# Performance work log

Hardware: AMD Instinct MI355X
Metric: run time of the kernel (lower is better)

The kernel has to match this reference:

```python
import jax, jax.numpy as jnp
import numpy as np

B, S, D = 8, 4096, 1024
MINR, MAXR = 0.9, 0.999


def setup_inputs() -> dict:
    key = jax.random.key(0)
    ks = jax.random.split(key, 10)

    def dense(k, fin, fout):
        # lecun_normal-style init for flax nn.Dense kernels
        return jax.random.normal(k, (fin, fout), jnp.float32) * (fin ** -0.5)

    x = jax.random.normal(ks[0], (B, S, D), jnp.float32)
    # RNN 'a' param: stable_init -> uniform in [min_rad, max_rad]
    a_fwd = jax.random.uniform(ks[1], (D,), jnp.float32, MINR, MAXR)
    # RGLRU 'a' param: recurrence_init
    u = jax.random.uniform(ks[2], (D,), jnp.float32)
    log_rad = 0.5 * jnp.log(u * (MAXR ** 2 - MINR ** 2) + MINR ** 2)
    a_param = jnp.log(jnp.exp(-log_rad) - 1.0)
    return {
        "x": x,
        "a_fwd": a_fwd,
        "Wf1": dense(ks[3], D, D), "bf1": jnp.zeros((D,), jnp.float32),
        "Wf2": dense(ks[4], D, D), "bf2": jnp.zeros((D,), jnp.float32),
        "Wbx": dense(ks[5], D, D), "bbx": jnp.zeros((D,), jnp.float32),
        "Wgx": dense(ks[6], D, D), "bgx": jnp.zeros((D,), jnp.float32),
        "Wga": dense(ks[7], D, D), "bga": jnp.zeros((D,), jnp.float32),
        "a_param": a_param,
        "Wb2": dense(ks[8], D, D), "bb2": jnp.zeros((D,), jnp.float32),
    }


def reference(x, a_fwd, Wf1, bf1, Wf2, bf2, Wbx, bbx, Wgx, bgx, Wga, bga,
              a_param, Wb2, bb2):
    b = x.shape[0]
    d = Wf1.shape[1]
    identity = x
    xg = jax.nn.gelu(x)  # flax nn.gelu default = tanh approximation

    # ---- forward branch: plain linear RNN  h = a*h + x_t ----
    u = xg @ Wf1 + bf1                       # [B,S,D]
    u_sf = jnp.swapaxes(u, 0, 1)             # [S,B,D]

    def step_f(h, ut):
        h = a_fwd * h + ut
        return h, h

    _, hf = jax.lax.scan(step_f, jnp.zeros((b, d), u.dtype), u_sf)
    out_f = jnp.swapaxes(hf, 0, 1) @ Wf2 + bf2

    # ---- backward branch: RG-LRU, reversed scan ----
    v = xg @ Wbx + bbx                       # [B,S,D]
    gate_x = jax.nn.sigmoid(v @ Wgx + bgx)
    gate_a = jax.nn.sigmoid(v @ Wga + bga)
    log_a = -8.0 * gate_a * jax.nn.softplus(a_param)
    a = jnp.exp(log_a)                       # [B,S,D]
    # h = a*h + sqrt(1 - a^2) * (gate_x * v)
    scaled_in = jnp.sqrt(1.0 - jnp.exp(2.0 * log_a)) * (gate_x * v)

    a_sf = jnp.swapaxes(a, 0, 1)             # [S,B,D]
    in_sf = jnp.swapaxes(scaled_in, 0, 1)    # [S,B,D]

    def step_b(h, inp):
        a_t, g_t = inp
        h = a_t * h + g_t
        return h, h

    _, hb = jax.lax.scan(step_b, jnp.zeros((b, d), v.dtype), (a_sf, in_sf),
                         reverse=True)
    out_b = jnp.swapaxes(hb, 0, 1) @ Wb2 + bb2

    return out_f + out_b + identity
```

## Files before the change

### kernel.cpp

```cpp
#include <hip/hip_runtime.h>

typedef __bf16 bf16;
typedef __bf16 bf16x8 __attribute__((ext_vector_type(8)));
typedef float floatx4 __attribute__((ext_vector_type(4)));

typedef __attribute__((address_space(1))) const void gvoid_t;
typedef __attribute__((address_space(3))) void lvoid_t;

#define B_DIM 8
#define S_DIM 4096
#define M_DIM 32768
#define CHUNK 128
#define NCHUNK 32

__device__ __forceinline__ void gload_lds16(const bf16* g, bf16* l) {
    __builtin_amdgcn_global_load_lds((gvoid_t*)g, (lvoid_t*)l, 16, 0, 0);
}

__device__ __forceinline__ float gelu_tanh(float x) {
    float x3 = x * x * x;
    return 0.5f * x * (1.0f + tanhf(0.7978845608028654f * (x + 0.044715f * x3)));
}

__device__ __forceinline__ float sigmoidf(float z) {
    return 1.0f / (1.0f + expf(-z));
}

__global__ void prep_weights(const float* __restrict__ W0, const float* __restrict__ W1,
                             const float* __restrict__ W2, const float* __restrict__ W3,
                             const float* __restrict__ W4, const float* __restrict__ W5,
                             bf16* __restrict__ T0, bf16* __restrict__ T1,
                             bf16* __restrict__ T2, bf16* __restrict__ T3,
                             bf16* __restrict__ T4, bf16* __restrict__ T5) {
    __shared__ float tile[32][33];
    int mz = blockIdx.z;
    const float* W = mz == 0 ? W0 : mz == 1 ? W1 : mz == 2 ? W2 : mz == 3 ? W3 : mz == 4 ? W4 : W5;
    bf16* T = mz == 0 ? T0 : mz == 1 ? T1 : mz == 2 ? T2 : mz == 3 ? T3 : mz == 4 ? T4 : T5;
    int tn = blockIdx.x * 32;
    int tk = blockIdx.y * 32;
    int tx = threadIdx.x & 31, ty = threadIdx.x >> 5;
#pragma unroll
    for (int i = 0; i < 4; ++i)
        tile[ty + i * 8][tx] = W[(size_t)(tk + ty + i * 8) * 1024 + tn + tx];
    __syncthreads();
#pragma unroll
    for (int i = 0; i < 4; ++i)
        T[(size_t)(tn + ty + i * 8) * 1024 + tk + tx] = (bf16)tile[tx][ty + i * 8];
}

__global__ void sp_kernel(const float* __restrict__ a_param, float* __restrict__ spbuf) {
    int d = blockIdx.x * 256 + threadIdx.x;
    spbuf[d] = log1pf(expf(a_param[d]));
}

__global__ void gelu_kernel(const float* __restrict__ x, bf16* __restrict__ xg) {
    size_t i = (size_t)blockIdx.x * 256 + threadIdx.x;
    float4 v = ((const float4*)x)[i];
    bf16 o0 = (bf16)gelu_tanh(v.x), o1 = (bf16)gelu_tanh(v.y);
    bf16 o2 = (bf16)gelu_tanh(v.z), o3 = (bf16)gelu_tanh(v.w);
    typedef __bf16 bf16x4 __attribute__((ext_vector_type(4)));
    bf16x4 o = {o0, o1, o2, o3};
    ((bf16x4*)xg)[i] = o;
}

template <int MODE>
__launch_bounds__(256, 2)
__global__ void gemm_k1024(const bf16* __restrict__ A, const bf16* __restrict__ Bt,
                           float* __restrict__ outf, bf16* __restrict__ outh,
                           const float* __restrict__ bias,
                           const float* __restrict__ auxf,
                           const bf16* __restrict__ labuf,
                           const bf16* __restrict__ vbuf,
                           const float* __restrict__ bias2) {
    __shared__ __align__(16) bf16 lsA[128 * 64];
    __shared__ __align__(16) bf16 lsB[128 * 64];
    const int tid = threadIdx.x;
    const int wave = tid >> 6;
    const int lane = tid & 63;
    const int lane15 = lane & 15;
    const int quad = lane >> 4;
    const int wm = wave & 1, wn = wave >> 1;
    const int blk = blockIdx.x;
    const int xcd = blk & 7;
    const int j = blk >> 3;
    const long m0 = (long)(xcd * 32 + (j >> 3)) * 128;
    const long n0 = (long)(j & 7) * 128;
    const int r_in = lane >> 3;
    const int cch = lane & 7;

    floatx4 acc[4][4] = {};

    for (int kt = 0; kt < 16; ++kt) {
        __syncthreads();
#pragma unroll
        for (int i = 0; i < 4; ++i) {
            int rr = (i * 4 + wave) * 8 + r_in;
            int g = cch ^ (rr & 7);
            gload_lds16(A + (size_t)(m0 + rr) * 1024 + kt * 64 + g * 8, &lsA[(i * 4 + wave) * 512]);
            gload_lds16(Bt + (size_t)(n0 + rr) * 1024 + kt * 64 + g * 8, &lsB[(i * 4 + wave) * 512]);
        }
        __syncthreads();
#pragma unroll
        for (int kk = 0; kk < 2; ++kk) {
            bf16x8 af[4], bfr[4];
#pragma unroll
            for (int mi = 0; mi < 4; ++mi) {
                int ml = wm * 64 + mi * 16 + lane15;
                af[mi] = *(const bf16x8*)&lsA[ml * 64 + ((kk * 4 + quad) ^ (ml & 7)) * 8];
            }
#pragma unroll
            for (int ni = 0; ni < 4; ++ni) {
                int nl = wn * 64 + ni * 16 + lane15;
                bfr[ni] = *(const bf16x8*)&lsB[nl * 64 + ((kk * 4 + quad) ^ (nl & 7)) * 8];
            }
#pragma unroll
            for (int mi = 0; mi < 4; ++mi)
#pragma unroll
                for (int ni = 0; ni < 4; ++ni)
                    acc[mi][ni] = __builtin_amdgcn_mfma_f32_16x16x32_bf16(af[mi], bfr[ni], acc[mi][ni], 0, 0, 0);
        }
    }

#pragma unroll
    for (int mi = 0; mi < 4; ++mi) {
#pragma unroll
        for (int ni = 0; ni < 4; ++ni) {
            floatx4 v = acc[mi][ni];
            long gn = n0 + wn * 64 + ni * 16 + lane15;
#pragma unroll
            for (int r = 0; r < 4; ++r) {
                long gm = m0 + wm * 64 + mi * 16 + quad * 4 + r;
                size_t o = (size_t)gm * 1024 + gn;
                if (MODE == 0) {
                    outf[o] = v[r] + bias[gn];
                } else if (MODE == 1) {
                    outh[o] = (bf16)(v[r] + bias[gn]);
                } else if (MODE == 2) {
                    float z = v[r] + bias[gn];
                    outh[o] = (bf16)(-8.0f * sigmoidf(z) * auxf[gn]);
                } else if (MODE == 3) {
                    float z = v[r] + bias[gn];
                    float laf = (float)labuf[o];
                    float sc = sqrtf(-expm1f(2.0f * laf)) * sigmoidf(z) * (float)vbuf[o];
                    outh[o] = (bf16)sc;
                } else if (MODE == 4) {
                    outf[o] = v[r] + bias[gn] + bias2[gn] + auxf[o];
                } else {
                    outf[o] += v[r];
                }
            }
        }
    }
}

__global__ void fscan1(const float* __restrict__ u, const float* __restrict__ a_fwd,
                       float* __restrict__ carry) {
    int d = (blockIdx.x & 3) * 256 + threadIdx.x;
    int c = (blockIdx.x >> 2) & 31;
    int b = blockIdx.x >> 7;
    float a = a_fwd[d];
    const float* up = u + ((size_t)(b * S_DIM + c * CHUNK)) * 1024 + d;
    float h = 0.0f;
#pragma unroll 8
    for (int t = 0; t < CHUNK; ++t) h = fmaf(a, h, up[(size_t)t * 1024]);
    carry[((size_t)c * 8 + b) * 1024 + d] = h;
}
__global__ void fscan2(const float* __restrict__ carry, const float* __restrict__ a_fwd,
                       float* __restrict__ H) {
    int idx = blockIdx.x * 256 + threadIdx.x;
    int d = idx & 1023, b = idx >> 10;
    float a = a_fwd[d];
    float aL = a;
#pragma unroll
    for (int i = 0; i < 7; ++i) aL *= aL;
    float h = 0.0f;
    for (int c = 0; c < NCHUNK; ++c) {
        size_t o = ((size_t)c * 8 + b) * 1024 + d;
        H[o] = h;
        h = fmaf(aL, h, carry[o]);
    }
}
__global__ void fscan3(const float* __restrict__ u, const float* __restrict__ a_fwd,
                       const float* __restrict__ H, bf16* __restrict__ hf) {
    int d = (blockIdx.x & 3) * 256 + threadIdx.x;
    int c = (blockIdx.x >> 2) & 31;
    int b = blockIdx.x >> 7;
    float a = a_fwd[d];
    const float* up = u + ((size_t)(b * S_DIM + c * CHUNK)) * 1024 + d;
    bf16* op = hf + ((size_t)(b * S_DIM + c * CHUNK)) * 1024 + d;
    float h = H[((size_t)c * 8 + b) * 1024 + d];
#pragma unroll 4
    for (int t = 0; t < CHUNK; ++t) {
        h = fmaf(a, h, up[(size_t)t * 1024]);
        op[(size_t)t * 1024] = (bf16)h;
    }
}

__global__ void bscan1(const bf16* __restrict__ la, const bf16* __restrict__ sc,
                       float* __restrict__ BL, float* __restrict__ BP) {
    int d = (blockIdx.x & 3) * 256 + threadIdx.x;
    int c = (blockIdx.x >> 2) & 31;
    int b = blockIdx.x >> 7;
    const bf16* lap = la + ((size_t)(b * S_DIM + c * CHUNK)) * 1024 + d;
    const bf16* gp = sc + ((size_t)(b * S_DIM + c * CHUNK)) * 1024 + d;
    float h = 0.0f, slog = 0.0f;
#pragma unroll 4
    for (int t = CHUNK - 1; t >= 0; --t) {
        float laf = (float)lap[(size_t)t * 1024];
        h = fmaf(expf(laf), h, (float)gp[(size_t)t * 1024]);
        slog += laf;
    }
    size_t o = ((size_t)c * 8 + b) * 1024 + d;
    BL[o] = h;
    BP[o] = expf(slog);
}
__global__ void bscan2(const float* __restrict__ BL, const float* __restrict__ BP,
                       float* __restrict__ R) {
    int idx = blockIdx.x * 256 + threadIdx.x;
    int d = idx & 1023, b = idx >> 10;
    float r = 0.0f;
    for (int c = NCHUNK - 1; c >= 0; --c) {
        size_t o = ((size_t)c * 8 + b) * 1024 + d;
        R[o] = r;
        r = fmaf(BP[o], r, BL[o]);
    }
}
__global__ void bscan3(const bf16* __restrict__ la, const bf16* __restrict__ sc,
                       const float* __restrict__ R, bf16* __restrict__ hb) {
    int d = (blockIdx.x & 3) * 256 + threadIdx.x;
    int c = (blockIdx.x >> 2) & 31;
    int b = blockIdx.x >> 7;
    const bf16* lap = la + ((size_t)(b * S_DIM + c * CHUNK)) * 1024 + d;
    const bf16* gp = sc + ((size_t)(b * S_DIM + c * CHUNK)) * 1024 + d;
    bf16* op = hb + ((size_t)(b * S_DIM + c * CHUNK)) * 1024 + d;
    float h = R[((size_t)c * 8 + b) * 1024 + d];
#pragma unroll 4
    for (int t = CHUNK - 1; t >= 0; --t) {
        h = fmaf(expf((float)lap[(size_t)t * 1024]), h, (float)gp[(size_t)t * 1024]);
        op[(size_t)t * 1024] = (bf16)h;
    }
}

extern "C" void kernel_launch(void* const* d_in, const int* in_sizes, int n_in,
                              void* d_out, int out_size, void* d_ws, size_t ws_size,
                              hipStream_t stream) {
    const float* x       = (const float*)d_in[0];
    const float* a_fwd   = (const float*)d_in[1];
    const float* Wf1     = (const float*)d_in[2];
    const float* bf1     = (const float*)d_in[3];
    const float* Wf2     = (const float*)d_in[4];
    const float* bf2     = (const float*)d_in[5];
    const float* Wbx     = (const float*)d_in[6];
    const float* bbx     = (const float*)d_in[7];
    const float* Wgx     = (const float*)d_in[8];
    const float* bgx     = (const float*)d_in[9];
    const float* Wga     = (const float*)d_in[10];
    const float* bga     = (const float*)d_in[11];
    const float* a_param = (const float*)d_in[12];
    const float* Wb2     = (const float*)d_in[13];
    const float* bb2     = (const float*)d_in[14];
    float* out = (float*)d_out;
    (void)in_sizes; (void)n_in; (void)out_size; (void)ws_size;

    char* ws = (char*)d_ws;
    size_t off = 0;
    const size_t WSZ = (size_t)1024 * 1024 * 2;
    bf16* Wf1t = (bf16*)(ws + off); off += WSZ;
    bf16* Wbxt = (bf16*)(ws + off); off += WSZ;
    bf16* Wgxt = (bf16*)(ws + off); off += WSZ;
    bf16* Wgat = (bf16*)(ws + off); off += WSZ;
    bf16* Wf2t = (bf16*)(ws + off); off += WSZ;
    bf16* Wb2t = (bf16*)(ws + off); off += WSZ;
    float* spbuf = (float*)(ws + off); off += 4096;
    const size_t BSZ = (size_t)M_DIM * 1024 * 2;
    bf16* buf0 = (bf16*)(ws + off); off += BSZ;
    bf16* buf1 = (bf16*)(ws + off); off += BSZ;
    bf16* buf2 = (bf16*)(ws + off); off += BSZ;
    float* Fc = (float*)(ws + off); off += (size_t)NCHUNK * 8 * 1024 * 4;
    float* FH = (float*)(ws + off); off += (size_t)NCHUNK * 8 * 1024 * 4;
    float* BL = (float*)(ws + off); off += (size_t)NCHUNK * 8 * 1024 * 4;
    float* BP = (float*)(ws + off); off += (size_t)NCHUNK * 8 * 1024 * 4;
    float* BR = (float*)(ws + off); off += (size_t)NCHUNK * 8 * 1024 * 4;

    bf16* xg = buf0;
    bf16* hf = buf0;
    bf16* vb = buf1;
    bf16* hb = buf1;
    bf16* la = buf2;
    float* u = (float*)d_out;
    bf16* sc = (bf16*)d_out;

    prep_weights<<<dim3(32, 32, 6), 256, 0, stream>>>(Wf1, Wbx, Wgx, Wga, Wf2, Wb2,
                                                      Wf1t, Wbxt, Wgxt, Wgat, Wf2t, Wb2t);
    sp_kernel<<<4, 256, 0, stream>>>(a_param, spbuf);
    gelu_kernel<<<32768, 256, 0, stream>>>(x, xg);
    gemm_k1024<0><<<2048, 256, 0, stream>>>(xg, Wf1t, u, nullptr, bf1, nullptr, nullptr, nullptr, nullptr);
    gemm_k1024<1><<<2048, 256, 0, stream>>>(xg, Wbxt, nullptr, vb, bbx, nullptr, nullptr, nullptr, nullptr);
    fscan1<<<1024, 256, 0, stream>>>(u, a_fwd, Fc);
    fscan2<<<32, 256, 0, stream>>>(Fc, a_fwd, FH);
    fscan3<<<1024, 256, 0, stream>>>(u, a_fwd, FH, hf);
    gemm_k1024<2><<<2048, 256, 0, stream>>>(vb, Wgat, nullptr, la, bga, spbuf, nullptr, nullptr, nullptr);
    gemm_k1024<3><<<2048, 256, 0, stream>>>(vb, Wgxt, nullptr, sc, bgx, nullptr, la, vb, nullptr);
    bscan1<<<1024, 256, 0, stream>>>(la, sc, BL, BP);
    bscan2<<<32, 256, 0, stream>>>(BL, BP, BR);
    bscan3<<<1024, 256, 0, stream>>>(la, sc, BR, hb);
    gemm_k1024<4><<<2048, 256, 0, stream>>>(hf, Wf2t, out, nullptr, bf2, x, nullptr, nullptr, bb2);
    gemm_k1024<5><<<2048, 256, 0, stream>>>(hb, Wb2t, out, nullptr, nullptr, nullptr, nullptr, nullptr, nullptr);
}
```

Baseline: 954.5 us.

## Replace GEMM with 256x256-tile, 8-wave, double-buffered prefetching kernel

All six bf16 GEMMs now use a new kernel with 256x256 output tiles and 512 threads (8 waves, each computing 128x64). LDS is double-buffered, and global-to-LDS loads for tile kt+2 are interleaved between four MFMA phases, using explicit waitcnt, barriers and setprio. The aim is more data reuse per tile and overlap of memory traffic with matrix math. In exchange it needs a much larger LDS footprint, which limits occupancy to about one block per CU, and it has fewer blocks to fill the GPU.

```diff
diff --git a/kernel.cpp b/kernel.cpp
--- a/kernel.cpp
+++ b/kernel.cpp
@@ -64,72 +64,144 @@
 }
 
 template <int MODE>
-__launch_bounds__(256, 2)
-__global__ void gemm_k1024(const bf16* __restrict__ A, const bf16* __restrict__ Bt,
-                           float* __restrict__ outf, bf16* __restrict__ outh,
-                           const float* __restrict__ bias,
-                           const float* __restrict__ auxf,
-                           const bf16* __restrict__ labuf,
-                           const bf16* __restrict__ vbuf,
-                           const float* __restrict__ bias2) {
-    __shared__ __align__(16) bf16 lsA[128 * 64];
-    __shared__ __align__(16) bf16 lsB[128 * 64];
+__launch_bounds__(512, 2)
+__global__ void gemm256(const bf16* __restrict__ A, const bf16* __restrict__ Bt,
+                        float* __restrict__ outf, bf16* __restrict__ outh,
+                        const float* __restrict__ bias,
+                        const float* __restrict__ auxf,
+                        const bf16* __restrict__ labuf,
+                        const bf16* __restrict__ vbuf,
+                        const float* __restrict__ bias2) {
+    __shared__ __align__(16) bf16 lsA[2][2][8192];
+    __shared__ __align__(16) bf16 lsB[2][2][8192];
     const int tid = threadIdx.x;
-    const int wave = tid >> 6;
-    const int lane = tid & 63;
-    const int lane15 = lane & 15;
-    const int quad = lane >> 4;
-    const int wm = wave & 1, wn = wave >> 1;
+    const int wave = tid >> 6, lane = tid & 63;
+    const int lane15 = lane & 15, quad = lane >> 4;
+    const int wm = wave >> 2;
+    const int wn = wave & 3;
+    const int bh = wn >> 1;
+    const int nrb = (wn & 1) * 4;
+
     const int blk = blockIdx.x;
-    const int xcd = blk & 7;
-    const int j = blk >> 3;
-    const long m0 = (long)(xcd * 32 + (j >> 3)) * 128;
-    const long n0 = (long)(j & 7) * 128;
-    const int r_in = lane >> 3;
-    const int cch = lane & 7;
-
-    floatx4 acc[4][4] = {};
+    const int j = (blk & 7) * 64 + (blk >> 3);
+    const long m0 = (long)(j >> 2) * 256;
+    const long n0 = (long)(j & 3) * 256;
+
+    const int sr = tid >> 3;
+    const int sk8 = (tid & 7) ^ (sr & 7);
+    const bf16* gA = A + (size_t)(m0 + sr) * 1024 + sk8 * 8;
+    const bf16* gB = Bt + (size_t)(n0 + sr) * 1024 + sk8 * 8;
+
+    floatx4 acc[8][4] = {};
+    bf16x8 af[4][2], b0[2][2], b1[2][2];
+
+    auto SA = [&](int buf, int half, int i, int kt) {
+        gload_lds16(gA + ((size_t)(half * 128 + i * 64)) * 1024 + kt * 64,
+                    &lsA[buf][half][i * 4096 + wave * 512]);
+    };
+    auto SB = [&](int buf, int half, int i, int kt) {
+        gload_lds16(gB + ((size_t)(half * 128 + i * 64)) * 1024 + kt * 64,
+                    &lsB[buf][half][i * 4096 + wave * 512]);
+    };
+    const int c0 = quad ^ (lane15 & 7);
+    auto LDA = [&](const bf16* h, int mi, int kk) -> bf16x8 {
+        return *(const bf16x8*)&h[(mi * 16 + lane15) * 64 + ((kk ? (c0 ^ 4) : c0)) * 8];
+    };
+    auto LDB = [&](const bf16* h, int ni, int kk) -> bf16x8 {
+        return *(const bf16x8*)&h[((nrb + ni) * 16 + lane15) * 64 + ((kk ? (c0 ^ 4) : c0)) * 8];
+    };
+
+    SA(0, 0, 0, 0); SA(0, 0, 1, 0); SA(0, 1, 0, 0); SA(0, 1, 1, 0);
+    SB(0, 0, 0, 0); SB(0, 0, 1, 0); SB(0, 1, 0, 0); SB(0, 1, 1, 0);
+    SA(1, 0, 0, 1); SA(1, 0, 1, 1); SA(1, 1, 0, 1); SA(1, 1, 1, 1);
+    SB(1, 0, 0, 1); SB(1, 0, 1, 1); SB(1, 1, 0, 1); SB(1, 1, 1, 1);
+    asm volatile("s_waitcnt vmcnt(8)" ::: "memory");
+    __builtin_amdgcn_s_barrier();
 
     for (int kt = 0; kt < 16; ++kt) {
-        __syncthreads();
-#pragma unroll
-        for (int i = 0; i < 4; ++i) {
-            int rr = (i * 4 + wave) * 8 + r_in;
-            int g = cch ^ (rr & 7);
-            gload_lds16(A + (size_t)(m0 + rr) * 1024 + kt * 64 + g * 8, &lsA[(i * 4 + wave) * 512]);
-            gload_lds16(Bt + (size_t)(n0 + rr) * 1024 + kt * 64 + g * 8, &lsB[(i * 4 + wave) * 512]);
-        }
-        __syncthreads();
-#pragma unroll
-        for (int kk = 0; kk < 2; ++kk) {
-            bf16x8 af[4], bfr[4];
-#pragma unroll
-            for (int mi = 0; mi < 4; ++mi) {
-                int ml = wm * 64 + mi * 16 + lane15;
-                af[mi] = *(const bf16x8*)&lsA[ml * 64 + ((kk * 4 + quad) ^ (ml & 7)) * 8];
-            }
-#pragma unroll
-            for (int ni = 0; ni < 4; ++ni) {
-                int nl = wn * 64 + ni * 16 + lane15;
-                bfr[ni] = *(const bf16x8*)&lsB[nl * 64 + ((kk * 4 + quad) ^ (nl & 7)) * 8];
-            }
-#pragma unroll
-            for (int mi = 0; mi < 4; ++mi)
-#pragma unroll
-                for (int ni = 0; ni < 4; ++ni)
-                    acc[mi][ni] = __builtin_amdgcn_mfma_f32_16x16x32_bf16(af[mi], bfr[ni], acc[mi][ni], 0, 0, 0);
-        }
-    }
-
-#pragma unroll
-    for (int mi = 0; mi < 4; ++mi) {
+        const int b = kt & 1;
+        const bf16* hA = &lsA[b][wm][0];
+        const bf16* hB = &lsB[b][bh][0];
+        const bool pf = (kt + 2 < 16);
+
+#pragma unroll
+        for (int mi = 0; mi < 4; ++mi) { af[mi][0] = LDA(hA, mi, 0); af[mi][1] = LDA(hA, mi, 1); }
+#pragma unroll
+        for (int ni = 0; ni < 2; ++ni) { b0[ni][0] = LDB(hB, ni, 0); b0[ni][1] = LDB(hB, ni, 1); }
+        asm volatile("s_waitcnt lgkmcnt(8)" ::: "memory");
+        __builtin_amdgcn_s_barrier();
+        asm volatile("s_waitcnt lgkmcnt(0)" ::: "memory");
+        __builtin_amdgcn_sched_barrier(0);
+        __builtin_amdgcn_s_setprio(1);
+#pragma unroll
+        for (int mi = 0; mi < 4; ++mi)
+#pragma unroll
+            for (int ni = 0; ni < 2; ++ni) {
+                acc[mi][ni] = __builtin_amdgcn_mfma_f32_16x16x32_bf16(af[mi][0], b0[ni][0], acc[mi][ni], 0, 0, 0);
+                acc[mi][ni] = __builtin_amdgcn_mfma_f32_16x16x32_bf16(af[mi][1], b0[ni][1], acc[mi][ni], 0, 0, 0);
+            }
+        __builtin_amdgcn_s_setprio(0);
+        __builtin_amdgcn_s_barrier();
+
+#pragma unroll
+        for (int ni = 0; ni < 2; ++ni) { b1[ni][0] = LDB(hB, 2 + ni, 0); b1[ni][1] = LDB(hB, 2 + ni, 1); }
+        if (pf) { SA(b, 0, 0, kt + 2); SA(b, 1, 0, kt + 2); }
+        __builtin_amdgcn_s_barrier();
+        asm volatile("s_waitcnt lgkmcnt(0)" ::: "memory");
+        __builtin_amdgcn_sched_barrier(0);
+        __builtin_amdgcn_s_setprio(1);
+#pragma unroll
+        for (int mi = 0; mi < 4; ++mi)
+#pragma unroll
+            for (int ni = 0; ni < 2; ++ni) {
+                acc[mi][2 + ni] = __builtin_amdgcn_mfma_f32_16x16x32_bf16(af[mi][0], b1[ni][0], acc[mi][2 + ni], 0, 0, 0);
+                acc[mi][2 + ni] = __builtin_amdgcn_mfma_f32_16x16x32_bf16(af[mi][1], b1[ni][1], acc[mi][2 + ni], 0, 0, 0);
+            }
+        __builtin_amdgcn_s_setprio(0);
+        __builtin_amdgcn_s_barrier();
+
+#pragma unroll
+        for (int mi = 0; mi < 4; ++mi) { af[mi][0] = LDA(hA, 4 + mi, 0); af[mi][1] = LDA(hA, 4 + mi, 1); }
+        if (pf) { SB(b, 0, 0, kt + 2); SB(b, 0, 1, kt + 2); SB(b, 1, 0, kt + 2); SB(b, 1, 1, kt + 2); }
+        __builtin_amdgcn_s_barrier();
+        asm volatile("s_waitcnt lgkmcnt(0)" ::: "memory");
+        __builtin_amdgcn_sched_barrier(0);
+        __builtin_amdgcn_s_setprio(1);
+#pragma unroll
+        for (int mi = 0; mi < 4; ++mi)
+#pragma unroll
+            for (int ni = 0; ni < 2; ++ni) {
+                acc[4 + mi][2 + ni] = __builtin_amdgcn_mfma_f32_16x16x32_bf16(af[mi][0], b1[ni][0], acc[4 + mi][2 + ni], 0, 0, 0);
+                acc[4 + mi][2 + ni] = __builtin_amdgcn_mfma_f32_16x16x32_bf16(af[mi][1], b1[ni][1], acc[4 + mi][2 + ni], 0, 0, 0);
+            }
+        __builtin_amdgcn_s_setprio(0);
+        __builtin_amdgcn_s_barrier();
+
+        if (pf) { SA(b, 0, 1, kt + 2); SA(b, 1, 1, kt + 2); }
+        __builtin_amdgcn_s_barrier();
+        __builtin_amdgcn_s_setprio(1);
+#pragma unroll
+        for (int mi = 0; mi < 4; ++mi)
+#pragma unroll
+            for (int ni = 0; ni < 2; ++ni) {
+                acc[4 + mi][ni] = __builtin_amdgcn_mfma_f32_16x16x32_bf16(af[mi][0], b0[ni][0], acc[4 + mi][ni], 0, 0, 0);
+                acc[4 + mi][ni] = __builtin_amdgcn_mfma_f32_16x16x32_bf16(af[mi][1], b0[ni][1], acc[4 + mi][ni], 0, 0, 0);
+            }
+        __builtin_amdgcn_s_setprio(0);
+        if (pf) { asm volatile("s_waitcnt vmcnt(8)" ::: "memory"); }
+        else    { asm volatile("s_waitcnt vmcnt(0)" ::: "memory"); }
+        __builtin_amdgcn_s_barrier();
+    }
+
+#pragma unroll
+    for (int mi = 0; mi < 8; ++mi) {
 #pragma unroll
         for (int ni = 0; ni < 4; ++ni) {
             floatx4 v = acc[mi][ni];
             long gn = n0 + wn * 64 + ni * 16 + lane15;
 #pragma unroll
             for (int r = 0; r < 4; ++r) {
-                long gm = m0 + wm * 64 + mi * 16 + quad * 4 + r;
+                long gm = m0 + wm * 128 + mi * 16 + quad * 4 + r;
                 size_t o = (size_t)gm * 1024 + gn;
                 if (MODE == 0) {
                     outf[o] = v[r] + bias[gn];
@@ -141,8 +213,8 @@
                 } else if (MODE == 3) {
                     float z = v[r] + bias[gn];
                     float laf = (float)labuf[o];
-                    float sc = sqrtf(-expm1f(2.0f * laf)) * sigmoidf(z) * (float)vbuf[o];
-                    outh[o] = (bf16)sc;
+                    float scv = sqrtf(-expm1f(2.0f * laf)) * sigmoidf(z) * (float)vbuf[o];
+                    outh[o] = (bf16)scv;
                 } else if (MODE == 4) {
                     outf[o] = v[r] + bias[gn] + bias2[gn] + auxf[o];
                 } else {
@@ -294,16 +366,16 @@
                                                       Wf1t, Wbxt, Wgxt, Wgat, Wf2t, Wb2t);
     sp_kernel<<<4, 256, 0, stream>>>(a_param, spbuf);
     gelu_kernel<<<32768, 256, 0, stream>>>(x, xg);
-    gemm_k1024<0><<<2048, 256, 0, stream>>>(xg, Wf1t, u, nullptr, bf1, nullptr, nullptr, nullptr, nullptr);
-    gemm_k1024<1><<<2048, 256, 0, stream>>>(xg, Wbxt, nullptr, vb, bbx, nullptr, nullptr, nullptr, nullptr);
+    gemm256<0><<<512, 512, 0, stream>>>(xg, Wf1t, u, nullptr, bf1, nullptr, nullptr, nullptr, nullptr);
+    gemm256<1><<<512, 512, 0, stream>>>(xg, Wbxt, nullptr, vb, bbx, nullptr, nullptr, nullptr, nullptr);
     fscan1<<<1024, 256, 0, stream>>>(u, a_fwd, Fc);
     fscan2<<<32, 256, 0, stream>>>(Fc, a_fwd, FH);
     fscan3<<<1024, 256, 0, stream>>>(u, a_fwd, FH, hf);
-    gemm_k1024<2><<<2048, 256, 0, stream>>>(vb, Wgat, nullptr, la, bga, spbuf, nullptr, nullptr, nullptr);
-    gemm_k1024<3><<<2048, 256, 0, stream>>>(vb, Wgxt, nullptr, sc, bgx, nullptr, la, vb, nullptr);
+    gemm256<2><<<512, 512, 0, stream>>>(vb, Wgat, nullptr, la, bga, spbuf, nullptr, nullptr, nullptr);
+    gemm256<3><<<512, 512, 0, stream>>>(vb, Wgxt, nullptr, sc, bgx, nullptr, la, vb, nullptr);
     bscan1<<<1024, 256, 0, stream>>>(la, sc, BL, BP);
     bscan2<<<32, 256, 0, stream>>>(BL, BP, BR);
     bscan3<<<1024, 256, 0, stream>>>(la, sc, BR, hb);
-    gemm_k1024<4><<<2048, 256, 0, stream>>>(hf, Wf2t, out, nullptr, bf2, x, nullptr, nullptr, bb2);
-    gemm_k1024<5><<<2048, 256, 0, stream>>>(hb, Wb2t, out, nullptr, nullptr, nullptr, nullptr, nullptr, nullptr);
-}
+    gemm256<4><<<512, 512, 0, stream>>>(hf, Wf2t, out, nullptr, bf2, x, nullptr, nullptr, bb2);
+    gemm256<5><<<512, 512, 0, stream>>>(hb, Wb2t, out, nullptr, nullptr, nullptr, nullptr, nullptr, nullptr);
+}
```

Result: slower. 1.026 ms (+7.5%).

## Fuse GEMM pairs sharing A operand and concatenate final output GEMMs along K

Applied to the files above, without the earlier changes.

The six separate K=1024 GEMMs become three kernels. The two GEMMs that read xg, and the two that read vb, each become a dual-B GEMM that loads the A tile once and accumulates two outputs. The two output projections become one K=2048 GEMM, which writes out once instead of doing a read-modify-write pass. This removes redundant A-tile loads, one full fp32 output round trip, the labuf reload and several launches. The cost is double the accumulator registers and 50% more LDS in the dual kernel, which could lower occupancy or cause spills under launch_bounds(256,2).

```diff
diff --git a/kernel.cpp b/kernel.cpp
--- a/kernel.cpp
+++ b/kernel.cpp
@@ -63,15 +63,103 @@
     ((bf16x4*)xg)[i] = o;
 }
 
-template <int MODE>
+template <int PAIR>
 __launch_bounds__(256, 2)
-__global__ void gemm_k1024(const bf16* __restrict__ A, const bf16* __restrict__ Bt,
-                           float* __restrict__ outf, bf16* __restrict__ outh,
-                           const float* __restrict__ bias,
-                           const float* __restrict__ auxf,
-                           const bf16* __restrict__ labuf,
-                           const bf16* __restrict__ vbuf,
-                           const float* __restrict__ bias2) {
+__global__ void gemm_dual(const bf16* __restrict__ A, const bf16* __restrict__ B0t,
+                          const bf16* __restrict__ B1t,
+                          float* __restrict__ outf, bf16* __restrict__ outh0,
+                          bf16* __restrict__ outh1,
+                          const float* __restrict__ bias0, const float* __restrict__ bias1,
+                          const float* __restrict__ sp, const bf16* __restrict__ vbuf) {
+    __shared__ __align__(16) bf16 lsA[128 * 64];
+    __shared__ __align__(16) bf16 lsB0[128 * 64];
+    __shared__ __align__(16) bf16 lsB1[128 * 64];
+    const int tid = threadIdx.x;
+    const int wave = tid >> 6;
+    const int lane = tid & 63;
+    const int lane15 = lane & 15;
+    const int quad = lane >> 4;
+    const int wm = wave & 1, wn = wave >> 1;
+    const int blk = blockIdx.x;
+    const int xcd = blk & 7;
+    const int j = blk >> 3;
+    const long m0 = (long)(xcd * 32 + (j >> 3)) * 128;
+    const long n0 = (long)(j & 7) * 128;
+    const int r_in = lane >> 3;
+    const int cch = lane & 7;
+
+    floatx4 acc0[4][4] = {};
+    floatx4 acc1[4][4] = {};
+
+    for (int kt = 0; kt < 16; ++kt) {
+        __syncthreads();
+#pragma unroll
+        for (int i = 0; i < 4; ++i) {
+            int rr = (i * 4 + wave) * 8 + r_in;
+            int g = cch ^ (rr & 7);
+            size_t ga = (size_t)(m0 + rr) * 1024 + kt * 64 + g * 8;
+            size_t gb = (size_t)(n0 + rr) * 1024 + kt * 64 + g * 8;
+            gload_lds16(A + ga, &lsA[(i * 4 + wave) * 512]);
+            gload_lds16(B0t + gb, &lsB0[(i * 4 + wave) * 512]);
+            gload_lds16(B1t + gb, &lsB1[(i * 4 + wave) * 512]);
+        }
+        __syncthreads();
+#pragma unroll
+        for (int kk = 0; kk < 2; ++kk) {
+            bf16x8 af[4], b0r[4], b1r[4];
+#pragma unroll
+            for (int mi = 0; mi < 4; ++mi) {
+                int ml = wm * 64 + mi * 16 + lane15;
+                af[mi] = *(const bf16x8*)&lsA[ml * 64 + ((kk * 4 + quad) ^ (ml & 7)) * 8];
+            }
+#pragma unroll
+            for (int ni = 0; ni < 4; ++ni) {
+                int nl = wn * 64 + ni * 16 + lane15;
+                int so = nl * 64 + ((kk * 4 + quad) ^ (nl & 7)) * 8;
+                b0r[ni] = *(const bf16x8*)&lsB0[so];
+                b1r[ni] = *(const bf16x8*)&lsB1[so];
+            }
+#pragma unroll
+            for (int mi = 0; mi < 4; ++mi)
+#pragma unroll
+                for (int ni = 0; ni < 4; ++ni) {
+                    acc0[mi][ni] = __builtin_amdgcn_mfma_f32_16x16x32_bf16(af[mi], b0r[ni], acc0[mi][ni], 0, 0, 0);
+                    acc1[mi][ni] = __builtin_amdgcn_mfma_f32_16x16x32_bf16(af[mi], b1r[ni], acc1[mi][ni], 0, 0, 0);
+                }
+        }
+    }
+
+#pragma unroll
+    for (int mi = 0; mi < 4; ++mi) {
+#pragma unroll
+        for (int ni = 0; ni < 4; ++ni) {
+            floatx4 v0 = acc0[mi][ni];
+            floatx4 v1 = acc1[mi][ni];
+            long gn = n0 + wn * 64 + ni * 16 + lane15;
+#pragma unroll
+            for (int r = 0; r < 4; ++r) {
+                long gm = m0 + wm * 64 + mi * 16 + quad * 4 + r;
+                size_t o = (size_t)gm * 1024 + gn;
+                if (PAIR == 0) {
+                    outf[o] = v0[r] + bias0[gn];
+                    outh1[o] = (bf16)(v1[r] + bias1[gn]);
+                } else {
+                    float laf = -8.0f * sigmoidf(v0[r] + bias0[gn]) * sp[gn];
+                    outh0[o] = (bf16)laf;
+                    float scv = sqrtf(-expm1f(2.0f * laf)) * sigmoidf(v1[r] + bias1[gn]) * (float)vbuf[o];
+                    outh1[o] = (bf16)scv;
+                }
+            }
+        }
+    }
+}
+
+__launch_bounds__(256, 2)
+__global__ void gemm_cat(const bf16* __restrict__ A0, const bf16* __restrict__ A1,
+                         const bf16* __restrict__ B0t, const bf16* __restrict__ B1t,
+                         float* __restrict__ outf,
+                         const float* __restrict__ bias0, const float* __restrict__ bias1,
+                         const float* __restrict__ xres) {
     __shared__ __align__(16) bf16 lsA[128 * 64];
     __shared__ __align__(16) bf16 lsB[128 * 64];
     const int tid = threadIdx.x;
@@ -90,14 +178,17 @@
 
     floatx4 acc[4][4] = {};
 
-    for (int kt = 0; kt < 16; ++kt) {
+    for (int kt = 0; kt < 32; ++kt) {
+        const bf16* Ap = (kt < 16) ? A0 : A1;
+        const bf16* Bp = (kt < 16) ? B0t : B1t;
+        const int ko = kt & 15;
         __syncthreads();
 #pragma unroll
         for (int i = 0; i < 4; ++i) {
             int rr = (i * 4 + wave) * 8 + r_in;
             int g = cch ^ (rr & 7);
-            gload_lds16(A + (size_t)(m0 + rr) * 1024 + kt * 64 + g * 8, &lsA[(i * 4 + wave) * 512]);
-            gload_lds16(Bt + (size_t)(n0 + rr) * 1024 + kt * 64 + g * 8, &lsB[(i * 4 + wave) * 512]);
+            gload_lds16(Ap + (size_t)(m0 + rr) * 1024 + ko * 64 + g * 8, &lsA[(i * 4 + wave) * 512]);
+            gload_lds16(Bp + (size_t)(n0 + rr) * 1024 + ko * 64 + g * 8, &lsB[(i * 4 + wave) * 512]);
         }
         __syncthreads();
 #pragma unroll
@@ -131,23 +222,7 @@
             for (int r = 0; r < 4; ++r) {
                 long gm = m0 + wm * 64 + mi * 16 + quad * 4 + r;
                 size_t o = (size_t)gm * 1024 + gn;
-                if (MODE == 0) {
-                    outf[o] = v[r] + bias[gn];
-                } else if (MODE == 1) {
-                    outh[o] = (bf16)(v[r] + bias[gn]);
-                } else if (MODE == 2) {
-                    float z = v[r] + bias[gn];
-                    outh[o] = (bf16)(-8.0f * sigmoidf(z) * auxf[gn]);
-                } else if (MODE == 3) {
-                    float z = v[r] + bias[gn];
-                    float laf = (float)labuf[o];
-                    float sc = sqrtf(-expm1f(2.0f * laf)) * sigmoidf(z) * (float)vbuf[o];
-                    outh[o] = (bf16)sc;
-                } else if (MODE == 4) {
-                    outf[o] = v[r] + bias[gn] + bias2[gn] + auxf[o];
-                } else {
-                    outf[o] += v[r];
-                }
+                outf[o] = v[r] + bias0[gn] + bias1[gn] + xres[o];
             }
         }
     }
@@ -294,16 +369,13 @@
                                                       Wf1t, Wbxt, Wgxt, Wgat, Wf2t, Wb2t);
     sp_kernel<<<4, 256, 0, stream>>>(a_param, spbuf);
     gelu_kernel<<<32768, 256, 0, stream>>>(x, xg);
-    gemm_k1024<0><<<2048, 256, 0, stream>>>(xg, Wf1t, u, nullptr, bf1, nullptr, nullptr, nullptr, nullptr);
-    gemm_k1024<1><<<2048, 256, 0, stream>>>(xg, Wbxt, nullptr, vb, bbx, nullptr, nullptr, nullptr, nullptr);
+    gemm_dual<0><<<2048, 256, 0, stream>>>(xg, Wf1t, Wbxt, u, nullptr, vb, bf1, bbx, nullptr, nullptr);
     fscan1<<<1024, 256, 0, stream>>>(u, a_fwd, Fc);
     fscan2<<<32, 256, 0, stream>>>(Fc, a_fwd, FH);
     fscan3<<<1024, 256, 0, stream>>>(u, a_fwd, FH, hf);
-    gemm_k1024<2><<<2048, 256, 0, stream>>>(vb, Wgat, nullptr, la, bga, spbuf, nullptr, nullptr, nullptr);
-    gemm_k1024<3><<<2048, 256, 0, stream>>>(vb, Wgxt, nullptr, sc, bgx, nullptr, la, vb, nullptr);
+    gemm_dual<1><<<2048, 256, 0, stream>>>(vb, Wgat, Wgxt, nullptr, la, sc, bga, bgx, spbuf, vb);
     bscan1<<<1024, 256, 0, stream>>>(la, sc, BL, BP);
     bscan2<<<32, 256, 0, stream>>>(BL, BP, BR);
     bscan3<<<1024, 256, 0, stream>>>(la, sc, BR, hb);
-    gemm_k1024<4><<<2048, 256, 0, stream>>>(hf, Wf2t, out, nullptr, bf2, x, nullptr, nullptr, bb2);
-    gemm_k1024<5><<<2048, 256, 0, stream>>>(hb, Wb2t, out, nullptr, nullptr, nullptr, nullptr, nullptr, nullptr);
-}
+    gemm_cat<<<2048, 256, 0, stream>>>(hf, hb, Wf2t, Wb2t, out, bf2, bb2, x);
+}
```

Result: no change. 940.9 us (-1.4%).
